# Kernel tuning notes

Measured on AMD Instinct MI355X. Metric: run time of the kernel, lower is better.

## Reference

```python
import jax, jax.numpy as jnp
import numpy as np

HIDDEN = 4096
N_HEADS = 32
N_KV_HEADS = 8
HEAD_DIM = HIDDEN // N_HEADS  # 128
ROPE_THETA = 10000.0


def rotate_half(x):
    x1, x2 = jnp.split(x, 2, axis=-1)
    return jnp.concatenate((-x2, x1), axis=-1)


def rope_cos_sin(seq_len, dim, theta, dtype):
    inv_freq = 1.0 / (theta ** (jnp.arange(0, dim, 2, dtype=jnp.float32) / dim))
    t = jnp.arange(seq_len, dtype=jnp.float32)
    freqs = jnp.outer(t, inv_freq)               # [S, D/2]
    emb = jnp.concatenate((freqs, freqs), axis=-1)  # [S, D]
    return jnp.cos(emb).astype(dtype), jnp.sin(emb).astype(dtype)


def setup_inputs() -> dict:
    key = jax.random.key(0)
    k0, k1, k2, k3, k4 = jax.random.split(key, 5)
    B, S = 1, 2048
    std = 1.0 / np.sqrt(HIDDEN)
    return {
        "hidden_states": jax.random.normal(k0, (B, S, HIDDEN), dtype=jnp.float32),
        "wq": jax.random.normal(k1, (N_HEADS * HEAD_DIM, HIDDEN), dtype=jnp.float32) * std,
        "wk": jax.random.normal(k2, (N_KV_HEADS * HEAD_DIM, HIDDEN), dtype=jnp.float32) * std,
        "wv": jax.random.normal(k3, (N_KV_HEADS * HEAD_DIM, HIDDEN), dtype=jnp.float32) * std,
        "wo": jax.random.normal(k4, (HIDDEN, N_HEADS * HEAD_DIM), dtype=jnp.float32) * std,
    }


def reference(hidden_states, wq, wk, wv, wo):
    B, S, _ = hidden_states.shape
    dtype = hidden_states.dtype
    G = N_HEADS // N_KV_HEADS  # query groups per kv head

    # projections (torch Linear: x @ W.T)
    q = (hidden_states @ wq.T).reshape(B, S, N_HEADS, HEAD_DIM).transpose(0, 2, 1, 3)      # [B,H,S,D]
    k = (hidden_states @ wk.T).reshape(B, S, N_KV_HEADS, HEAD_DIM).transpose(0, 2, 1, 3)   # [B,Hkv,S,D]
    v = (hidden_states @ wv.T).reshape(B, S, N_KV_HEADS, HEAD_DIM).transpose(0, 2, 1, 3)   # [B,Hkv,S,D]

    cos, sin = rope_cos_sin(S, HEAD_DIM, ROPE_THETA, dtype)  # [S,D]
    cos = cos[None, None]  # [1,1,S,D]
    sin = sin[None, None]
    q = q * cos + rotate_half(q) * sin
    k = k * cos + rotate_half(k) * sin

    # GQA: group query heads with their kv head (equivalent to repeat_interleave on kv)
    qg = q.reshape(B, N_KV_HEADS, G, S, HEAD_DIM)
    scale = 1.0 / np.sqrt(HEAD_DIM)
    scores = jnp.einsum("bkgsd,bktd->bkgst", qg, k) * scale  # [B,Hkv,G,S,S]

    causal = jnp.tril(jnp.ones((S, S), dtype=bool))
    scores = jnp.where(causal, scores, -jnp.inf)
    probs = jax.nn.softmax(scores.astype(jnp.float32), axis=-1).astype(dtype)

    out = jnp.einsum("bkgst,bktd->bkgsd", probs, v)  # [B,Hkv,G,S,D]
    out = out.reshape(B, N_HEADS, S, HEAD_DIM).transpose(0, 2, 1, 3).reshape(B, S, N_HEADS * HEAD_DIM)
    return out @ wo.T
```

## Files before the change

### kernel.cpp

```cpp
#include <hip/hip_runtime.h>
#include <hip/hip_bf16.h>


typedef _Float16 half4_t __attribute__((ext_vector_type(4)));
typedef _Float16 half8_t __attribute__((ext_vector_type(8)));
typedef float f32x4 __attribute__((ext_vector_type(4)));

#define S_LEN 2048
#define HID 4096
#define NH 32
#define NKV 8

__device__ __forceinline__ void gload_lds16(const void* g, void* l) {
  __builtin_amdgcn_global_load_lds((const __attribute__((address_space(1))) void*)g,
                                   (__attribute__((address_space(3))) void*)l, 16, 0, 0);
}

__global__ __launch_bounds__(256) void cvt_f32_f16(const float* __restrict__ src,
                                                   _Float16* __restrict__ dst, int n4) {
  int i = blockIdx.x * 256 + threadIdx.x;
  if (i >= n4) return;
  f32x4 v = *(const f32x4*)(src + (size_t)i * 4);
  half4_t h = {(_Float16)v[0], (_Float16)v[1], (_Float16)v[2], (_Float16)v[3]};
  *(half4_t*)(dst + (size_t)i * 4) = h;
}

__global__ __launch_bounds__(256) void cvt_qkv(const float* __restrict__ wq,
                                               const float* __restrict__ wk,
                                               const float* __restrict__ wv,
                                               _Float16* __restrict__ dst, int n4) {
  int i = blockIdx.x * 256 + threadIdx.x;
  if (i >= n4) return;
  size_t e = (size_t)i * 4;
  const float* src;
  size_t off;
  if (e < (size_t)4096 * 4096)      { src = wq; off = e; }
  else if (e < (size_t)5120 * 4096) { src = wk; off = e - (size_t)4096 * 4096; }
  else                              { src = wv; off = e - (size_t)5120 * 4096; }
  f32x4 v = *(const f32x4*)(src + off);
  half4_t h = {(_Float16)v[0], (_Float16)v[1], (_Float16)v[2], (_Float16)v[3]};
  *(half4_t*)(dst + e) = h;
}

__global__ __launch_bounds__(256) void rope_table_kernel(float* __restrict__ cost,
                                                         float* __restrict__ sint) {
  int i = blockIdx.x * 256 + threadIdx.x;
  int d = i & 63;
  int s = i >> 6;
  float inv = exp2f(-(float)d * (13.287712379549449f / 64.0f));
  float f = (float)s * inv;
  cost[i] = cosf(f);
  sint[i] = sinf(f);
}

__global__ __launch_bounds__(256) void rope_apply_q(_Float16* __restrict__ X,
                                                    const float* __restrict__ cost,
                                                    const float* __restrict__ sint) {
  int idx = blockIdx.x * 256 + threadIdx.x;
  int g = idx & 15;
  int tmp = idx >> 4;
  int h = tmp % NH;
  int s = tmp / NH;
  int d0 = g * 4;
  size_t base = (size_t)s * HID + h * 128 + d0;
  half4_t x1 = *(half4_t*)(X + base);
  half4_t x2 = *(half4_t*)(X + base + 64);
  const float* cp = cost + s * 64 + d0;
  const float* sp = sint + s * 64 + d0;
  half4_t y1, y2;
#pragma unroll
  for (int j = 0; j < 4; ++j) {
    float c = cp[j], sn = sp[j];
    float a = (float)x1[j], b = (float)x2[j];
    y1[j] = (_Float16)(a * c - b * sn);
    y2[j] = (_Float16)(b * c + a * sn);
  }
  *(half4_t*)(X + base) = y1;
  *(half4_t*)(X + base + 64) = y2;
}

__global__ __launch_bounds__(256) void rope_k2_inplace(_Float16* __restrict__ K2,
                                                       const float* __restrict__ cost,
                                                       const float* __restrict__ sint) {
  int idx = blockIdx.x * 256 + threadIdx.x;
  int g = idx & 15;
  int tmp = idx >> 4;
  int h = tmp % NKV;
  int s = tmp / NKV;
  int d0 = g * 4;
  size_t tb = (size_t)h * (S_LEN * 128) + (size_t)(s >> 4) * 2048 + (size_t)(s & 15) * 8;
  size_t a1 = tb + (size_t)(d0 >> 3) * 128 + (d0 & 7);
  size_t a2 = a1 + 1024;
  half4_t x1 = *(half4_t*)(K2 + a1);
  half4_t x2 = *(half4_t*)(K2 + a2);
  const float* cp = cost + s * 64 + d0;
  const float* sp = sint + s * 64 + d0;
  half4_t y1, y2;
#pragma unroll
  for (int j = 0; j < 4; ++j) {
    float c = cp[j], sn = sp[j];
    float a = (float)x1[j], b = (float)x2[j];
    y1[j] = (_Float16)(a * c - b * sn);
    y2[j] = (_Float16)(b * c + a * sn);
  }
  *(half4_t*)(K2 + a1) = y1;
  *(half4_t*)(K2 + a2) = y2;
}

template <int MODE>
__global__ __launch_bounds__(256) void gemmT(const _Float16* __restrict__ A,
                                             const _Float16* __restrict__ W,
                                             void* __restrict__ out,
                                             _Float16* __restrict__ K2,
                                             _Float16* __restrict__ V2) {
  const int id = blockIdx.x;
  const int xcd = id & 7, slot = id >> 3;
  const int c = (MODE == 0) ? (xcd * 6 + (slot >> 4)) : (xcd * 4 + (slot >> 4));
  const int m0 = (slot & 15) * 128;
  const int col0 = c * 128;
  __shared__ __align__(16) _Float16 As[3][128 * 32];
  __shared__ __align__(16) _Float16 Bs[3][128 * 32];
  const int t = threadIdx.x, w = t >> 6, l = t & 63, lr = l & 15, lg = l >> 4;
  const int wm = (w >> 1) * 64, wn = (w & 1) * 64;
  const int srow = l >> 2;
  const int scolS = (((l & 3) ^ ((l >> 3) & 3))) * 8;
  const int rc = (lr >> 1) & 3;
  const _Float16* ap = A + (size_t)m0 * 4096 + scolS;
  const _Float16* bp = W + (size_t)col0 * 4096 + scolS;

  f32x4 acc[4][4] = {};

#define STAGE(buf_, kb_)                                              \
  _Pragma("unroll") for (int it = 0; it < 2; ++it) {                  \
    const int ci = it * 4 + w;                                        \
    const int r = ci * 16 + srow;                                     \
    gload_lds16(ap + (size_t)r * 4096 + (kb_), &As[buf_][ci * 512]);  \
    gload_lds16(bp + (size_t)r * 4096 + (kb_), &Bs[buf_][ci * 512]);  \
  }

  STAGE(0, 0)
  STAGE(1, 32)

  for (int k = 0; k < 128; ++k) {
    const int kb2 = (k + 2) * 32;
    const int buf = k % 3;
    __builtin_amdgcn_s_barrier();
    __builtin_amdgcn_sched_barrier(0);
    if (kb2 < 4096) {
      STAGE((k + 2) % 3, kb2)
      asm volatile("s_waitcnt vmcnt(4)" ::: "memory");
    } else {
      asm volatile("s_waitcnt vmcnt(0)" ::: "memory");
    }
    __builtin_amdgcn_sched_barrier(0);
    __builtin_amdgcn_s_barrier();
    half8_t af[4], bf[4];
#pragma unroll
    for (int mi = 0; mi < 4; ++mi)
      af[mi] = *(const half8_t*)&As[buf][(wm + mi * 16 + lr) * 32 + (lg ^ rc) * 8];
#pragma unroll
    for (int ni = 0; ni < 4; ++ni)
      bf[ni] = *(const half8_t*)&Bs[buf][(wn + ni * 16 + lr) * 32 + (lg ^ rc) * 8];
#pragma unroll
    for (int mi = 0; mi < 4; ++mi)
#pragma unroll
      for (int ni = 0; ni < 4; ++ni)
        acc[mi][ni] = __builtin_amdgcn_mfma_f32_16x16x32_f16(af[mi], bf[ni], acc[mi][ni], 0, 0, 0);
  }
#undef STAGE

#pragma unroll
  for (int mi = 0; mi < 4; ++mi) {
#pragma unroll
    for (int ni = 0; ni < 4; ++ni) {
      const int row = m0 + wm + mi * 16 + lg * 4;
      const int col = col0 + wn + ni * 16 + lr;
      if (MODE == 1) {
#pragma unroll
        for (int i = 0; i < 4; ++i)
          ((float*)out)[(size_t)(row + i) * 4096 + col] = acc[mi][ni][i];
      } else {
        if (col < 4096) {
#pragma unroll
          for (int i = 0; i < 4; ++i)
            ((_Float16*)out)[(size_t)(row + i) * 4096 + col] = (_Float16)acc[mi][ni][i];
        } else if (col < 5120) {
          const int cl = col - 4096;
          const int h = cl >> 7, d = cl & 127;
          const size_t kk = (size_t)h * (S_LEN * 128) + (size_t)(row >> 4) * 2048 +
                            (size_t)(d >> 3) * 128 + (d & 7);
#pragma unroll
          for (int i = 0; i < 4; ++i)
            K2[kk + ((row + i) & 15) * 8] = (_Float16)acc[mi][ni][i];
        } else {
          const int cl = col - 5120;
          half4_t o;
#pragma unroll
          for (int i = 0; i < 4; ++i) o[i] = (_Float16)acc[mi][ni][i];
          *(half4_t*)(V2 + (size_t)(cl >> 7) * (S_LEN * 128) + (size_t)(row >> 4) * 2048 +
                      (size_t)(cl & 127) * 16 + (row & 15)) = o;
        }
      }
    }
  }
}

__global__ __launch_bounds__(256) void attn_kernel(const _Float16* __restrict__ Q,
                                                   const _Float16* __restrict__ K2,
                                                   const _Float16* __restrict__ V2,
                                                   _Float16* __restrict__ Op,
                                                   float* __restrict__ Md) {
  const int bid = blockIdx.x;
  const int hk = bid & 7;
  const int split = (bid >> 3) & 1;
  const int qt = 63 - (bid >> 4);
  const int w = threadIdx.x >> 6;
  const int h = hk * 4 + w;
  const int l = threadIdx.x & 63;
  const int lr = l & 15;
  const int lg = l >> 4;
  const float scale = 0.08838834764831845f;
  const float LOG2E = 1.4426950408889634f;
  const float NEG = -1.0e30f;

  const int half_steps = qt + 1;
  const int kt0 = split * half_steps;
  const int kt1 = kt0 + half_steps;

  int sq[2];
  half8_t qf[2][4];
#pragma unroll
  for (int qc = 0; qc < 2; ++qc) {
    sq[qc] = qt * 32 + qc * 16 + lr;
#pragma unroll
    for (int c = 0; c < 4; ++c)
      qf[qc][c] = *(const half8_t*)(Q + (size_t)sq[qc] * HID + h * 128 + c * 32 + lg * 8);
  }
  const _Float16* Kb = K2 + (size_t)hk * (S_LEN * 128);
  const _Float16* Vb = V2 + (size_t)hk * (S_LEN * 128);

  f32x4 acc[8][2] = {};
  float m[2] = {NEG, NEG};
  float den[2] = {0.f, 0.f};

  for (int kt = kt0; kt < kt1; ++kt) {
    half8_t kf[4];
#pragma unroll
    for (int c = 0; c < 4; ++c)
      kf[c] = *(const half8_t*)(Kb + (size_t)kt * 2048 + (c * 4 + lg) * 128 + lr * 8);
    f32x4 s0 = {0.f, 0.f, 0.f, 0.f}, s1 = {0.f, 0.f, 0.f, 0.f};
#pragma unroll
    for (int c = 0; c < 4; ++c) {
      s0 = __builtin_amdgcn_mfma_f32_16x16x32_f16(kf[c], qf[0][c], s0, 0, 0, 0);
      s1 = __builtin_amdgcn_mfma_f32_16x16x32_f16(kf[c], qf[1][c], s1, 0, 0, 0);
    }
    const int kbase = kt * 16 + lg * 4;
    float sc[2][4];
#pragma unroll
    for (int i = 0; i < 4; ++i) {
      sc[0][i] = s0[i] * scale;
      sc[1][i] = s1[i] * scale;
    }
    if (kt >= 2 * qt) {
#pragma unroll
      for (int qc = 0; qc < 2; ++qc)
#pragma unroll
        for (int i = 0; i < 4; ++i)
          if (kbase + i > sq[qc]) sc[qc][i] = NEG;
    }
    half4_t pf[2];
#pragma unroll
    for (int qc = 0; qc < 2; ++qc) {
      float mx = fmaxf(fmaxf(sc[qc][0], sc[qc][1]), fmaxf(sc[qc][2], sc[qc][3]));
      mx = fmaxf(mx, __shfl_xor(mx, 16));
      mx = fmaxf(mx, __shfl_xor(mx, 32));
      if (!__all(mx - m[qc] <= 8.0f)) {
        float mn = fmaxf(m[qc], mx);
        float corr = exp2f((m[qc] - mn) * LOG2E);
        den[qc] *= corr;
#pragma unroll
        for (int dc = 0; dc < 8; ++dc)
#pragma unroll
          for (int i = 0; i < 4; ++i) acc[dc][qc][i] *= corr;
        m[qc] = mn;
      }
      float ps = 0.f, p[4];
#pragma unroll
      for (int i = 0; i < 4; ++i) {
        p[i] = exp2f((sc[qc][i] - m[qc]) * LOG2E);
        ps += p[i];
      }
      ps += __shfl_xor(ps, 16);
      ps += __shfl_xor(ps, 32);
      den[qc] += ps;
      pf[qc] = (half4_t){(_Float16)p[0], (_Float16)p[1], (_Float16)p[2], (_Float16)p[3]};
    }
#pragma unroll
    for (int dc = 0; dc < 8; ++dc) {
      half4_t vf = *(const half4_t*)(Vb + (size_t)kt * 2048 + (dc * 16 + lr) * 16 + lg * 4);
      acc[dc][0] = __builtin_amdgcn_mfma_f32_16x16x16f16(vf, pf[0], acc[dc][0], 0, 0, 0);
      acc[dc][1] = __builtin_amdgcn_mfma_f32_16x16x16f16(vf, pf[1], acc[dc][1], 0, 0, 0);
    }
  }

  _Float16* Os = Op + (size_t)split * S_LEN * HID;
#pragma unroll
  for (int qc = 0; qc < 2; ++qc) {
    float inv = den[qc] > 0.f ? 1.0f / den[qc] : 0.f;
#pragma unroll
    for (int dc = 0; dc < 8; ++dc) {
      half4_t o;
#pragma unroll
      for (int i = 0; i < 4; ++i) o[i] = (_Float16)(acc[dc][qc][i] * inv);
      *(half4_t*)(Os + (size_t)sq[qc] * HID + h * 128 + dc * 16 + lg * 4) = o;
    }
    if (lg == 0) {
      int mdix = ((split * S_LEN + sq[qc]) * NH + h) * 2;
      Md[mdix] = m[qc];
      Md[mdix + 1] = den[qc];
    }
  }
}

__global__ __launch_bounds__(256) void attn_combine(const _Float16* __restrict__ Op,
                                                    const float* __restrict__ Md,
                                                    _Float16* __restrict__ O) {
  const float LOG2E = 1.4426950408889634f;
  int idx = blockIdx.x * 256 + threadIdx.x;
  int dd = (idx & 15) * 8;
  int h = (idx >> 4) & 31;
  int s = idx >> 9;
  int base = (s * NH + h) * 2;
  float m0 = Md[base], den0 = Md[base + 1];
  float m1 = Md[S_LEN * NH * 2 + base], den1 = Md[S_LEN * NH * 2 + base + 1];
  float M = fmaxf(m0, m1);
  float w0 = den0 * exp2f((m0 - M) * LOG2E);
  float w1 = den1 * exp2f((m1 - M) * LOG2E);
  float r = 1.0f / (w0 + w1);
  w0 *= r;
  w1 *= r;
  size_t off = (size_t)s * HID + h * 128 + dd;
  half8_t a = *(const half8_t*)(Op + off);
  half8_t b = *(const half8_t*)(Op + (size_t)S_LEN * HID + off);
  half8_t o;
#pragma unroll
  for (int j = 0; j < 8; ++j) o[j] = (_Float16)(w0 * (float)a[j] + w1 * (float)b[j]);
  *(half8_t*)(O + off) = o;
}

extern "C" void kernel_launch(void* const* d_in, const int* in_sizes, int n_in,
                              void* d_out, int out_size, void* d_ws, size_t ws_size,
                              hipStream_t stream) {
  (void)in_sizes; (void)n_in; (void)out_size; (void)ws_size;
  const float* hs = (const float*)d_in[0];
  const float* wq = (const float*)d_in[1];
  const float* wk = (const float*)d_in[2];
  const float* wv = (const float*)d_in[3];
  const float* wo = (const float*)d_in[4];

  char* ws = (char*)d_ws;
  _Float16* hs_h = (_Float16*)(ws);
  _Float16* q_h  = (_Float16*)(ws + (16u << 20));
  _Float16* K2   = (_Float16*)(ws + (32u << 20));
  _Float16* V2   = (_Float16*)(ws + (36u << 20));
  float* cost    = (float*)(ws + (40u << 20));
  float* sint    = (float*)(ws + (40u << 20) + (512u << 10));
  _Float16* wqkv = (_Float16*)(ws + (41u << 20));
  _Float16* Op   = wqkv;
  float* Md      = (float*)(ws + (73u << 20));
  _Float16* wo_h = wqkv;
  _Float16* o_h  = hs_h;

  cvt_f32_f16<<<8192, 256, 0, stream>>>(hs, hs_h, (S_LEN * HID) / 4);
  rope_table_kernel<<<(S_LEN * 64) / 256, 256, 0, stream>>>(cost, sint);
  cvt_qkv<<<24576, 256, 0, stream>>>(wq, wk, wv, wqkv, (6144 * 4096) / 4);

  gemmT<0><<<768, 256, 0, stream>>>(hs_h, wqkv, q_h, K2, V2);

  rope_apply_q<<<(S_LEN * NH * 16) / 256, 256, 0, stream>>>(q_h, cost, sint);
  rope_k2_inplace<<<(S_LEN * NKV * 16) / 256, 256, 0, stream>>>(K2, cost, sint);

  attn_kernel<<<1024, 256, 0, stream>>>(q_h, K2, V2, Op, Md);
  attn_combine<<<4096, 256, 0, stream>>>(Op, Md, o_h);

  cvt_f32_f16<<<16384, 256, 0, stream>>>(wo, wo_h, (HID * HID) / 4);
  gemmT<1><<<512, 256, 0, stream>>>(o_h, wo_h, d_out, nullptr, nullptr);
}
```

Baseline: 385.5 us.

## Fuse fp32-to-fp16 weight conversion into GEMM B-operand loading

Removes the separate weight conversion kernels for Wqkv and Wo, and has the GEMM load fp32 weight tiles into registers, convert them to fp16 and write them swizzled into LDS inside the pipelined k-loop. This avoids writing and re-reading the fp16 weight copy in global memory and drops two kernel launches. In exchange each GEMM block reads fp32 weights, twice the bytes per tile, and reads them repeatedly across the 16 M-tiles. It also adds register staging and LDS-write work to the main loop, which may reduce how well loads overlap with the MFMA work.

```diff
diff --git a/kernel.cpp b/kernel.cpp
--- a/kernel.cpp
+++ b/kernel.cpp
@@ -23,23 +23,6 @@
   f32x4 v = *(const f32x4*)(src + (size_t)i * 4);
   half4_t h = {(_Float16)v[0], (_Float16)v[1], (_Float16)v[2], (_Float16)v[3]};
   *(half4_t*)(dst + (size_t)i * 4) = h;
-}
-
-__global__ __launch_bounds__(256) void cvt_qkv(const float* __restrict__ wq,
-                                               const float* __restrict__ wk,
-                                               const float* __restrict__ wv,
-                                               _Float16* __restrict__ dst, int n4) {
-  int i = blockIdx.x * 256 + threadIdx.x;
-  if (i >= n4) return;
-  size_t e = (size_t)i * 4;
-  const float* src;
-  size_t off;
-  if (e < (size_t)4096 * 4096)      { src = wq; off = e; }
-  else if (e < (size_t)5120 * 4096) { src = wk; off = e - (size_t)4096 * 4096; }
-  else                              { src = wv; off = e - (size_t)5120 * 4096; }
-  f32x4 v = *(const f32x4*)(src + off);
-  half4_t h = {(_Float16)v[0], (_Float16)v[1], (_Float16)v[2], (_Float16)v[3]};
-  *(half4_t*)(dst + e) = h;
 }
 
 __global__ __launch_bounds__(256) void rope_table_kernel(float* __restrict__ cost,
@@ -108,8 +91,10 @@
 }
 
 template <int MODE>
-__global__ __launch_bounds__(256) void gemmT(const _Float16* __restrict__ A,
-                                             const _Float16* __restrict__ W,
+__global__ __launch_bounds__(256) void gemmD(const _Float16* __restrict__ A,
+                                             const float* __restrict__ W0,
+                                             const float* __restrict__ W1,
+                                             const float* __restrict__ W2,
                                              void* __restrict__ out,
                                              _Float16* __restrict__ K2,
                                              _Float16* __restrict__ V2) {
@@ -118,6 +103,15 @@
   const int c = (MODE == 0) ? (xcd * 6 + (slot >> 4)) : (xcd * 4 + (slot >> 4));
   const int m0 = (slot & 15) * 128;
   const int col0 = c * 128;
+  const float* Wsel;
+  int colLoc;
+  if (MODE == 0) {
+    if (col0 < 4096)      { Wsel = W0; colLoc = col0; }
+    else if (col0 < 5120) { Wsel = W1; colLoc = col0 - 4096; }
+    else                  { Wsel = W2; colLoc = col0 - 5120; }
+  } else {
+    Wsel = W0; colLoc = col0;
+  }
   __shared__ __align__(16) _Float16 As[3][128 * 32];
   __shared__ __align__(16) _Float16 Bs[3][128 * 32];
   const int t = threadIdx.x, w = t >> 6, l = t & 63, lr = l & 15, lg = l >> 4;
@@ -126,32 +120,55 @@
   const int scolS = (((l & 3) ^ ((l >> 3) & 3))) * 8;
   const int rc = (lr >> 1) & 3;
   const _Float16* ap = A + (size_t)m0 * 4096 + scolS;
-  const _Float16* bp = W + (size_t)col0 * 4096 + scolS;
+  const float* bw = Wsel + (size_t)colLoc * 4096;
 
   f32x4 acc[4][4] = {};
-
-#define STAGE(buf_, kb_)                                              \
+  f32x4 br[4];
+
+#define GLOADA(buf_, kb_)                                             \
   _Pragma("unroll") for (int it = 0; it < 2; ++it) {                  \
     const int ci = it * 4 + w;                                        \
     const int r = ci * 16 + srow;                                     \
     gload_lds16(ap + (size_t)r * 4096 + (kb_), &As[buf_][ci * 512]);  \
-    gload_lds16(bp + (size_t)r * 4096 + (kb_), &Bs[buf_][ci * 512]);  \
-  }
-
-  STAGE(0, 0)
-  STAGE(1, 32)
+  }
+#define LOADB(kb_)                                                    \
+  _Pragma("unroll") for (int it = 0; it < 4; ++it) {                  \
+    const int r = it * 32 + (t >> 3);                                 \
+    br[it] = *(const f32x4*)(bw + (size_t)r * 4096 + (kb_) + (t & 7) * 4); \
+  }
+#define CVTW(buf_)                                                    \
+  _Pragma("unroll") for (int it = 0; it < 4; ++it) {                  \
+    const int r = it * 32 + (t >> 3);                                 \
+    half4_t h;                                                        \
+    _Pragma("unroll") for (int j = 0; j < 4; ++j) h[j] = (_Float16)br[it][j]; \
+    const int fc = (t & 7) >> 1;                                      \
+    *(half4_t*)&Bs[buf_][r * 32 + ((fc ^ ((r >> 1) & 3)) * 8) + (t & 1) * 4] = h; \
+  }
+
+  LOADB(0)
+  GLOADA(0, 0)
+  asm volatile("s_waitcnt vmcnt(2)" ::: "memory");
+  __builtin_amdgcn_sched_barrier(0);
+  CVTW(0)
+  LOADB(32)
+  GLOADA(1, 32)
+  asm volatile("s_waitcnt lgkmcnt(0)" ::: "memory");
+  __builtin_amdgcn_sched_barrier(0);
 
   for (int k = 0; k < 128; ++k) {
-    const int kb2 = (k + 2) * 32;
     const int buf = k % 3;
     __builtin_amdgcn_s_barrier();
+    asm volatile("s_waitcnt vmcnt(2)" ::: "memory");
     __builtin_amdgcn_sched_barrier(0);
-    if (kb2 < 4096) {
-      STAGE((k + 2) % 3, kb2)
-      asm volatile("s_waitcnt vmcnt(4)" ::: "memory");
-    } else {
+    if (k + 1 < 128) { CVTW((k + 1) % 3) }
+    if (k + 2 < 128) {
+      LOADB((k + 2) * 32)
+      GLOADA((k + 2) % 3, (k + 2) * 32)
+      asm volatile("s_waitcnt vmcnt(6)" ::: "memory");
+    } else if (k == 127) {
       asm volatile("s_waitcnt vmcnt(0)" ::: "memory");
     }
+    asm volatile("s_waitcnt lgkmcnt(0)" ::: "memory");
     __builtin_amdgcn_sched_barrier(0);
     __builtin_amdgcn_s_barrier();
     half8_t af[4], bf[4];
@@ -167,7 +184,9 @@
       for (int ni = 0; ni < 4; ++ni)
         acc[mi][ni] = __builtin_amdgcn_mfma_f32_16x16x32_f16(af[mi], bf[ni], acc[mi][ni], 0, 0, 0);
   }
-#undef STAGE
+#undef GLOADA
+#undef LOADB
+#undef CVTW
 
 #pragma unroll
   for (int mi = 0; mi < 4; ++mi) {
@@ -365,17 +384,14 @@
   _Float16* V2   = (_Float16*)(ws + (36u << 20));
   float* cost    = (float*)(ws + (40u << 20));
   float* sint    = (float*)(ws + (40u << 20) + (512u << 10));
-  _Float16* wqkv = (_Float16*)(ws + (41u << 20));
-  _Float16* Op   = wqkv;
+  _Float16* Op   = (_Float16*)(ws + (41u << 20));
   float* Md      = (float*)(ws + (73u << 20));
-  _Float16* wo_h = wqkv;
   _Float16* o_h  = hs_h;
 
   cvt_f32_f16<<<8192, 256, 0, stream>>>(hs, hs_h, (S_LEN * HID) / 4);
   rope_table_kernel<<<(S_LEN * 64) / 256, 256, 0, stream>>>(cost, sint);
-  cvt_qkv<<<24576, 256, 0, stream>>>(wq, wk, wv, wqkv, (6144 * 4096) / 4);
-
-  gemmT<0><<<768, 256, 0, stream>>>(hs_h, wqkv, q_h, K2, V2);
+
+  gemmD<0><<<768, 256, 0, stream>>>(hs_h, wq, wk, wv, q_h, K2, V2);
 
   rope_apply_q<<<(S_LEN * NH * 16) / 256, 256, 0, stream>>>(q_h, cost, sint);
   rope_k2_inplace<<<(S_LEN * NKV * 16) / 256, 256, 0, stream>>>(K2, cost, sint);
@@ -383,6 +399,5 @@
   attn_kernel<<<1024, 256, 0, stream>>>(q_h, K2, V2, Op, Md);
   attn_combine<<<4096, 256, 0, stream>>>(Op, Md, o_h);
 
-  cvt_f32_f16<<<16384, 256, 0, stream>>>(wo, wo_h, (HID * HID) / 4);
-  gemmT<1><<<512, 256, 0, stream>>>(o_h, wo_h, d_out, nullptr, nullptr);
-}
+  gemmD<1><<<512, 256, 0, stream>>>(o_h, wo, nullptr, nullptr, d_out, nullptr, nullptr);
+}
```

After: 437.9 us. +13.6%, slower.
